# Kernel optimization log

Measured on AMD Instinct MI355X. Metric: run time of the kernel, lower is better.

## Reference

```python
import jax, jax.numpy as jnp
import numpy as np

B, L, C, H = 4, 2048, 1024, 16
D = C // H  # head dim = 64


def setup_inputs() -> dict:
    key = jax.random.key(0)
    ks = jax.random.split(key, 7)
    x = jax.random.normal(ks[0], (B, L, C), dtype=jnp.float32)
    Wqkv = jax.random.normal(ks[1], (C, 3 * C), dtype=jnp.float32) * 0.02
    bqkv = jnp.zeros((3 * C,), dtype=jnp.float32)
    gamma_q = jnp.ones((H, D), dtype=jnp.float32)
    gamma_k = jnp.ones((H, D), dtype=jnp.float32)
    Wout = jax.random.normal(ks[2], (C, C), dtype=jnp.float32) * 0.02
    bout = jnp.zeros((C,), dtype=jnp.float32)
    return {"x": x, "Wqkv": Wqkv, "bqkv": bqkv, "gamma_q": gamma_q,
            "gamma_k": gamma_k, "Wout": Wout, "bout": bout}


def _multihead_rms_norm(t, gamma):
    # SparseMultiHeadRMSNorm: L2-normalize last dim (F.normalize), * gamma * sqrt(D)
    norm = jnp.maximum(jnp.linalg.norm(t, axis=-1, keepdims=True), 1e-12)
    return (t / norm) * gamma * jnp.sqrt(jnp.float32(D))


def reference(x, Wqkv, bqkv, gamma_q, gamma_k, Wout, bout):
    # qkv projection: [B,L,C] -> [B,L,3,H,D]
    qkv = (x @ Wqkv + bqkv).reshape(B, L, 3, H, D)
    q, k, v = qkv[:, :, 0], qkv[:, :, 1], qkv[:, :, 2]
    # qk rms norm (gamma broadcasts over [B,L,H,D])
    q = _multihead_rms_norm(q, gamma_q)
    k = _multihead_rms_norm(k, gamma_k)
    # full scaled dot product attention within each grid (batch element)
    scale = 1.0 / jnp.sqrt(jnp.float32(D))
    scores = jnp.einsum('bqhd,bkhd->bhqk', q, k) * scale
    attn = jax.nn.softmax(scores, axis=-1)
    h = jnp.einsum('bhqk,bkhd->bqhd', attn, v).reshape(B, L, C)
    return h @ Wout + bout
```

## Files before the change

### kernel.cpp

```cpp
#include <hip/hip_runtime.h>
#include <math.h>

#define BB 4
#define LL 2048
#define CC 1024
#define HH 16
#define DD 64
#define MM (BB * LL)

typedef float f32x4 __attribute__((ext_vector_type(4)));
typedef short short8 __attribute__((ext_vector_type(8)));
typedef unsigned short ushort_t;
typedef unsigned long long u64_t;

#define MFMA_BF16(A, B, C) __builtin_amdgcn_mfma_f32_16x16x32_bf16(A, B, C, 0, 0, 0)

#define QSCALE 0.180336880f

__device__ __forceinline__ unsigned short f2bf(float x) {
    unsigned int u = __float_as_uint(x);
    u += 0x7fffu + ((u >> 16) & 1u);
    return (unsigned short)(u >> 16);
}

__device__ __forceinline__ unsigned pack_bf2(float a, float b) {
#if __has_builtin(__builtin_amdgcn_perm)
    return __builtin_amdgcn_perm(__float_as_uint(b) + 0x8000u,
                                 __float_as_uint(a) + 0x8000u, 0x07060302u);
#else
    return ((__float_as_uint(b) + 0x8000u) & 0xFFFF0000u) |
           ((__float_as_uint(a) + 0x8000u) >> 16);
#endif
}

__device__ __forceinline__ float fast_exp2(float x) {
#if __has_builtin(__builtin_amdgcn_exp2f)
    return __builtin_amdgcn_exp2f(x);
#else
    return exp2f(x);
#endif
}

__global__ __launch_bounds__(256)
void prep_all(const float* __restrict__ x, ushort_t* __restrict__ xh,
              const float* __restrict__ Wq, ushort_t* __restrict__ Tq,
              const float* __restrict__ Wo, ushort_t* __restrict__ To)
{
    __shared__ float sT[64][65];
    int bid = blockIdx.x;
    const int tid = threadIdx.x;

    if (bid < 4096) {
        const int i = (bid * 256 + tid) * 8;
        f32x4 a = *(const f32x4*)(x + i);
        f32x4 b = *(const f32x4*)(x + i + 4);
        short8 h;
#pragma unroll
        for (int j = 0; j < 4; ++j) {
            h[j]     = (short)f2bf(a[j]);
            h[4 + j] = (short)f2bf(b[j]);
        }
        *(short8*)(xh + i) = h;
        return;
    }
    bid -= 4096;

    const float* W;
    ushort_t* T;
    int N, bx, by;
    if (bid < 768) { W = Wq; T = Tq; N = 3 * CC; bx = bid % 48; by = bid / 48; }
    else { bid -= 768; W = Wo; T = To; N = CC; bx = bid % 16; by = bid / 16; }

    const int K = CC;
    const int k0 = by * 64, n0 = bx * 64;
    const int r = tid >> 2, c0 = (tid & 3) * 16;

    const float* wp = W + (size_t)(k0 + r) * N + n0 + c0;
#pragma unroll
    for (int u = 0; u < 4; ++u) {
        f32x4 v = *(const f32x4*)(wp + 4 * u);
        sT[r][c0 + 4 * u + 0] = v[0];
        sT[r][c0 + 4 * u + 1] = v[1];
        sT[r][c0 + 4 * u + 2] = v[2];
        sT[r][c0 + 4 * u + 3] = v[3];
    }
    __syncthreads();

    const int nn = tid >> 2, kk0 = (tid & 3) * 16;
    short8 h0, h1;
#pragma unroll
    for (int u = 0; u < 8; ++u) {
        h0[u] = (short)f2bf(sT[kk0 + u][nn]);
        h1[u] = (short)f2bf(sT[kk0 + 8 + u][nn]);
    }
    ushort_t* oh = T + (size_t)(n0 + nn) * K + k0 + kk0;
    *(short8*)oh = h0; *(short8*)(oh + 8) = h1;
}

__global__ __launch_bounds__(256, 3)
void gemm_qkv(const ushort_t* __restrict__ Agh,
              const ushort_t* __restrict__ Bh,
              const float* __restrict__ bias,
              const float* __restrict__ gq, const float* __restrict__ gk,
              ushort_t* __restrict__ Qbh,
              ushort_t* __restrict__ Kh,
              ushort_t* __restrict__ Vth)
{
    __shared__ ushort_t smem[16384];
    ushort_t* sAh = smem;
    ushort_t* sBh = smem + 8192;

    const int K = CC, lda = CC, nbx = (3 * CC) / 128;

    const int nwg = gridDim.x;
    const int cpx = nwg >> 3;
    const int id  = blockIdx.x;
    const int swz = (id & 7) * cpx + (id >> 3);
    const int bx = swz % nbx, by = swz / nbx;
    const int m0 = by * 128, n0 = bx * 128;

    const int tid  = threadIdx.x;
    const int lane = tid & 63;
    const int wv   = tid >> 6;
    const int l4   = lane >> 4, l16 = lane & 15;
    const int wm   = wv >> 1,  wn  = wv & 1;

    const int r0  = tid >> 2;
    const int c0  = (tid & 3) * 16;
    const int ch0 = c0 >> 3;

    f32x4 acc[4][4];
#pragma unroll
    for (int i = 0; i < 4; ++i)
#pragma unroll
        for (int j = 0; j < 4; ++j) acc[i][j] = 0.f;

    short8 stgA[4], stgB[4];
#pragma unroll
    for (int it = 0; it < 2; ++it) {
        const ushort_t* ahp = Agh + (size_t)(m0 + r0 + 64 * it) * lda + c0;
        stgA[2 * it]     = *(const short8*)(ahp);
        stgA[2 * it + 1] = *(const short8*)(ahp + 8);
        const ushort_t* bhp = Bh + (size_t)(n0 + r0 + 64 * it) * K + c0;
        stgB[2 * it]     = *(const short8*)(bhp);
        stgB[2 * it + 1] = *(const short8*)(bhp + 8);
    }

    for (int kt = 0; kt < K; kt += 64) {
        __syncthreads();
#pragma unroll
        for (int it = 0; it < 2; ++it) {
            const int row  = r0 + 64 * it;
            const int sA   = row & 7;
            const int base = row * 64;
            const int cA = ((ch0) ^ sA) * 8, cB = ((ch0 + 1) ^ sA) * 8;
            *(short8*)&sAh[base + cA] = stgA[2 * it];
            *(short8*)&sAh[base + cB] = stgA[2 * it + 1];
            *(short8*)&sBh[base + cA] = stgB[2 * it];
            *(short8*)&sBh[base + cB] = stgB[2 * it + 1];
        }
        __syncthreads();

        if (kt + 64 < K) {
#pragma unroll
            for (int it = 0; it < 2; ++it) {
                const ushort_t* ahp = Agh + (size_t)(m0 + r0 + 64 * it) * lda + kt + 64 + c0;
                stgA[2 * it]     = *(const short8*)(ahp);
                stgA[2 * it + 1] = *(const short8*)(ahp + 8);
                const ushort_t* bhp = Bh + (size_t)(n0 + r0 + 64 * it) * K + kt + 64 + c0;
                stgB[2 * it]     = *(const short8*)(bhp);
                stgB[2 * it + 1] = *(const short8*)(bhp + 8);
            }
        }

#pragma unroll
        for (int ks = 0; ks < 2; ++ks) {
            const int chf = (((ks << 2) | l4) ^ (l16 & 7)) * 8;
            short8 fbh[4];
#pragma unroll
            for (int j = 0; j < 4; ++j) {
                const int idx = (64 * wn + 16 * j + l16) * 64 + chf;
                fbh[j] = *(const short8*)&sBh[idx];
            }
#pragma unroll
            for (int i = 0; i < 4; ++i) {
                const int idx = (64 * wm + 16 * i + l16) * 64 + chf;
                short8 fah = *(const short8*)&sAh[idx];
#pragma unroll
                for (int j = 0; j < 4; ++j)
                    acc[i][j] = MFMA_BF16(fah, fbh[j], acc[i][j]);
            }
        }
    }

    const int region = n0 >> 10;
    float bv[4];
#pragma unroll
    for (int j = 0; j < 4; ++j) bv[j] = bias[n0 + 64 * wn + 16 * j + l16];
#pragma unroll
    for (int i = 0; i < 4; ++i)
#pragma unroll
        for (int j = 0; j < 4; ++j)
#pragma unroll
            for (int r = 0; r < 4; ++r) acc[i][j][r] += bv[j];

    const int b = m0 >> 11;

    if (region < 2) {
        const int hloc = ((n0 & 1023) >> 6) + wn;
        const float* g = (region == 0 ? gq : gk) + hloc * DD;
        float gv[4];
#pragma unroll
        for (int j = 0; j < 4; ++j) gv[j] = g[16 * j + l16];
#pragma unroll
        for (int i = 0; i < 4; ++i)
#pragma unroll
        for (int r = 0; r < 4; ++r) {
            float ss = 0.f;
#pragma unroll
            for (int j = 0; j < 4; ++j) ss += acc[i][j][r] * acc[i][j][r];
#pragma unroll
            for (int off = 1; off < 16; off <<= 1) ss += __shfl_xor(ss, off);
            const float s = 8.0f / fmaxf(sqrtf(ss), 1e-12f);
#pragma unroll
            for (int j = 0; j < 4; ++j) acc[i][j][r] *= s * gv[j];
        }

        if (region == 0) {
#pragma unroll
            for (int i = 0; i < 4; ++i)
#pragma unroll
            for (int r = 0; r < 4; ++r) {
                const int row = m0 + 64 * wm + 16 * i + 4 * l4 + r;
                ushort_t* op = Qbh + (size_t)row * CC + n0 + 64 * wn + l16;
#pragma unroll
                for (int j = 0; j < 4; ++j)
                    op[16 * j] = f2bf(acc[i][j][r] * QSCALE);
            }
        } else {
            const int hk = ((n0 - 1024) >> 6) + wn;
#pragma unroll
            for (int i = 0; i < 4; ++i)
#pragma unroll
            for (int r = 0; r < 4; ++r) {
                const int l = (m0 & 2047) + 64 * wm + 16 * i + 4 * l4 + r;
                const size_t base = ((size_t)(b * HH + hk) * LL + l) * DD + l16;
#pragma unroll
                for (int j = 0; j < 4; ++j)
                    Kh[base + 16 * j] = f2bf(acc[i][j][r]);
            }
        }
    } else {
        __syncthreads();
        ushort_t* vh = smem;
#pragma unroll
        for (int i = 0; i < 4; ++i)
#pragma unroll
        for (int r = 0; r < 4; ++r) {
            const int lr = 64 * wm + 16 * i + 4 * l4 + r;
#pragma unroll
            for (int j = 0; j < 4; ++j) {
                const int c = 64 * wn + 16 * j + l16;
                vh[lr * 128 + c] = f2bf(acc[i][j][r]);
            }
        }
        __syncthreads();
        const int c    = tid & 127;
        const int half = tid >> 7;
        const int hv   = ((n0 - 2048) >> 6) + (c >> 6);
        const int d    = c & 63;
        ushort_t* oh = Vth + ((size_t)(b * HH + hv) * DD + d) * LL + (m0 & 2047) + half * 64;
#pragma unroll
        for (int u = 0; u < 8; ++u) {
            const int l0 = half * 64 + u * 8;
            short8 hv8;
#pragma unroll
            for (int e = 0; e < 8; ++e)
                hv8[e] = (short)vh[(l0 + e) * 128 + c];
            *(short8*)&oh[u * 8] = hv8;
        }
    }
}

__global__ __launch_bounds__(256, 3)
void gemm_out1(const ushort_t* __restrict__ Ah,
               const ushort_t* __restrict__ Bh,
               const float* __restrict__ bias, float* __restrict__ Cg)
{
    __shared__ ushort_t sAh[8192];
    __shared__ ushort_t sBh[8192];

    const int K = CC, nbx = CC / 128;

    const int nwg = gridDim.x;
    const int cpx = nwg >> 3;
    const int id  = blockIdx.x;
    const int sw  = (id & 7) * cpx + (id >> 3);
    const int bx = sw % nbx, by = sw / nbx;
    const int m0 = by * 128, n0 = bx * 128;

    const int tid  = threadIdx.x;
    const int lane = tid & 63;
    const int wv   = tid >> 6;
    const int l4   = lane >> 4, l16 = lane & 15;
    const int wm   = wv >> 1,  wn  = wv & 1;

    const int r0  = tid >> 2;
    const int c0  = (tid & 3) * 16;
    const int ch0 = c0 >> 3;

    f32x4 acc[4][4];
#pragma unroll
    for (int i = 0; i < 4; ++i)
#pragma unroll
        for (int j = 0; j < 4; ++j) acc[i][j] = 0.f;

    short8 stgA[4], stgB[4];
#pragma unroll
    for (int it = 0; it < 2; ++it) {
        const ushort_t* ahp = Ah + (size_t)(m0 + r0 + 64 * it) * CC + c0;
        stgA[2 * it]     = *(const short8*)(ahp);
        stgA[2 * it + 1] = *(const short8*)(ahp + 8);
        const ushort_t* bhp = Bh + (size_t)(n0 + r0 + 64 * it) * K + c0;
        stgB[2 * it]     = *(const short8*)(bhp);
        stgB[2 * it + 1] = *(const short8*)(bhp + 8);
    }

    for (int kt = 0; kt < K; kt += 64) {
        __syncthreads();
#pragma unroll
        for (int it = 0; it < 2; ++it) {
            const int row  = r0 + 64 * it;
            const int sA   = row & 7;
            const int base = row * 64;
            const int cA = ((ch0) ^ sA) * 8, cB = ((ch0 + 1) ^ sA) * 8;
            *(short8*)&sAh[base + cA] = stgA[2 * it];
            *(short8*)&sAh[base + cB] = stgA[2 * it + 1];
            *(short8*)&sBh[base + cA] = stgB[2 * it];
            *(short8*)&sBh[base + cB] = stgB[2 * it + 1];
        }
        __syncthreads();

        if (kt + 64 < K) {
#pragma unroll
            for (int it = 0; it < 2; ++it) {
                const ushort_t* ahp = Ah + (size_t)(m0 + r0 + 64 * it) * CC + kt + 64 + c0;
                stgA[2 * it]     = *(const short8*)(ahp);
                stgA[2 * it + 1] = *(const short8*)(ahp + 8);
                const ushort_t* bhp = Bh + (size_t)(n0 + r0 + 64 * it) * K + kt + 64 + c0;
                stgB[2 * it]     = *(const short8*)(bhp);
                stgB[2 * it + 1] = *(const short8*)(bhp + 8);
            }
        }

#pragma unroll
        for (int ks = 0; ks < 2; ++ks) {
            const int chf = (((ks << 2) | l4) ^ (l16 & 7)) * 8;
            short8 fbh[4];
#pragma unroll
            for (int j = 0; j < 4; ++j) {
                const int idx = (64 * wn + 16 * j + l16) * 64 + chf;
                fbh[j] = *(const short8*)&sBh[idx];
            }
#pragma unroll
            for (int i = 0; i < 4; ++i) {
                const int idx = (64 * wm + 16 * i + l16) * 64 + chf;
                short8 fah = *(const short8*)&sAh[idx];
#pragma unroll
                for (int j = 0; j < 4; ++j)
                    acc[i][j] = MFMA_BF16(fah, fbh[j], acc[i][j]);
            }
        }
    }

    float bv[4];
#pragma unroll
    for (int j = 0; j < 4; ++j) bv[j] = bias[n0 + 64 * wn + 16 * j + l16];
#pragma unroll
    for (int i = 0; i < 4; ++i)
#pragma unroll
    for (int r = 0; r < 4; ++r) {
        const int row = m0 + 64 * wm + 16 * i + 4 * l4 + r;
        float* cp = Cg + (size_t)row * CC + n0 + 64 * wn + l16;
#pragma unroll
        for (int j = 0; j < 4; ++j) cp[16 * j] = acc[i][j][r] + bv[j];
    }
}

__global__ __launch_bounds__(256, 2)
void flash11(const ushort_t* __restrict__ Qbh,
             const ushort_t* __restrict__ Kh,
             const ushort_t* __restrict__ Vth,
             ushort_t* __restrict__ Hb)
{
    __shared__ ushort_t sKh[4096], sVh[4096];
    __shared__ ushort_t sP[4][64 * 68];

    const int i    = blockIdx.x;
    const int xcd  = i & 7;
    const int slot = i >> 3;
    const int qt   = slot & 7;
    const int bh   = ((slot >> 3) << 3) | xcd;
    const int b    = bh >> 4, h = bh & 15;

    const int tid  = threadIdx.x;
    const int lane = tid & 63;
    const int wv   = tid >> 6;
    const int l4   = lane >> 4, l16 = lane & 15;

    short8 qh[4][2];
    const int qr0 = qt * 256 + wv * 64;
#pragma unroll
    for (int qf = 0; qf < 4; ++qf)
#pragma unroll
    for (int sl = 0; sl < 2; ++sl)
        qh[qf][sl] = *(const short8*)(Qbh + (size_t)(b * LL + qr0 + qf * 16 + l16) * CC
                                      + h * DD + sl * 32 + l4 * 8);

    short8 ones;
#pragma unroll
    for (int j = 0; j < 8; ++j) ones[j] = (short)0x3F80;

    f32x4 O[4][4];
    f32x4 acc_l[4];
#pragma unroll
    for (int qf = 0; qf < 4; ++qf) {
        acc_l[qf] = 0.f;
#pragma unroll
        for (int t = 0; t < 4; ++t) O[qf][t] = 0.f;
    }

    const int r_ = tid >> 2;
    const int c2 = (tid & 3) * 2;

    short8 stg[4];
    {
        const size_t kgb = ((size_t)bh * LL + r_) * DD + c2 * 8;
        const size_t vgb = ((size_t)bh * DD + r_) * LL + c2 * 8;
        stg[0] = *(const short8*)&Kh[kgb];  stg[1] = *(const short8*)&Kh[kgb + 8];
        stg[2] = *(const short8*)&Vth[vgb]; stg[3] = *(const short8*)&Vth[vgb + 8];
    }

    for (int kt = 0; kt < LL / 64; ++kt) {
        __syncthreads();
        {
            const int wr = r_ * 64, s = r_ & 7;
            const int cA = ((c2) ^ s) * 8, cB = ((c2 + 1) ^ s) * 8;
            *(short8*)&sKh[wr + cA] = stg[0];
            *(short8*)&sKh[wr + cB] = stg[1];
            *(short8*)&sVh[wr + cA] = stg[2];
            *(short8*)&sVh[wr + cB] = stg[3];
        }
        __syncthreads();
        if (kt + 1 < LL / 64) {
            const size_t kgb = ((size_t)bh * LL + (kt + 1) * 64 + r_) * DD + c2 * 8;
            const size_t vgb = ((size_t)bh * DD + r_) * LL + (kt + 1) * 64 + c2 * 8;
            stg[0] = *(const short8*)&Kh[kgb];  stg[1] = *(const short8*)&Kh[kgb + 8];
            stg[2] = *(const short8*)&Vth[vgb]; stg[3] = *(const short8*)&Vth[vgb + 8];
        }

        f32x4 S[4][4];
#pragma unroll
        for (int qf = 0; qf < 4; ++qf)
#pragma unroll
        for (int t = 0; t < 4; ++t) S[qf][t] = 0.f;

        __builtin_amdgcn_s_setprio(1);
#pragma unroll
        for (int t = 0; t < 4; ++t) {
            const int row = 16 * t + l16;
            const int swr = row & 7;
#pragma unroll
            for (int sl = 0; sl < 2; ++sl) {
                const int idx = row * 64 + (((sl << 2) | l4) ^ swr) * 8;
                short8 kh8 = *(const short8*)&sKh[idx];
#pragma unroll
                for (int qf = 0; qf < 4; ++qf)
                    S[qf][t] = MFMA_BF16(kh8, qh[qf][sl], S[qf][t]);
            }
        }
        __builtin_amdgcn_s_setprio(0);

#pragma unroll
        for (int qf = 0; qf < 4; ++qf)
#pragma unroll
        for (int t = 0; t < 4; ++t)
#pragma unroll
            for (int r = 0; r < 4; ++r)
                S[qf][t][r] = fast_exp2(S[qf][t][r]);

#pragma unroll
        for (int qf = 0; qf < 4; ++qf)
#pragma unroll
        for (int t = 0; t < 4; ++t) {
            unsigned lo = pack_bf2(S[qf][t][0], S[qf][t][1]);
            unsigned hi = pack_bf2(S[qf][t][2], S[qf][t][3]);
            const int widx = (qf * 16 + l16) * 68 + 16 * t + 4 * l4;
            *(u64_t*)&sP[wv][widx] = (u64_t)lo | ((u64_t)hi << 32);
        }
        asm volatile("s_waitcnt lgkmcnt(0)" ::: "memory");
        __builtin_amdgcn_sched_barrier(0);

        short8 pa[4][2];
#pragma unroll
        for (int qf = 0; qf < 4; ++qf)
#pragma unroll
        for (int sl = 0; sl < 2; ++sl) {
            const int ridx = (qf * 16 + l16) * 68 + sl * 32 + 8 * l4;
            union { u64_t q[2]; short8 s8; } u;
            u.q[0] = *(const u64_t*)&sP[wv][ridx];
            u.q[1] = *(const u64_t*)&sP[wv][ridx + 4];
            pa[qf][sl] = u.s8;
        }

        __builtin_amdgcn_s_setprio(1);
#pragma unroll
        for (int qf = 0; qf < 4; ++qf) {
            acc_l[qf] = MFMA_BF16(pa[qf][0], ones, acc_l[qf]);
            acc_l[qf] = MFMA_BF16(pa[qf][1], ones, acc_l[qf]);
        }
#pragma unroll
        for (int dt = 0; dt < 4; ++dt) {
            const int row = 16 * dt + l16;
            const int swr = row & 7;
#pragma unroll
            for (int sl = 0; sl < 2; ++sl) {
                const int idx = row * 64 + (((sl << 2) | l4) ^ swr) * 8;
                short8 vh8 = *(const short8*)&sVh[idx];
#pragma unroll
                for (int qf = 0; qf < 4; ++qf)
                    O[qf][dt] = MFMA_BF16(pa[qf][sl], vh8, O[qf][dt]);
            }
        }
        __builtin_amdgcn_s_setprio(0);
    }

#pragma unroll
    for (int qf = 0; qf < 4; ++qf) {
        f32x4 iv;
#pragma unroll
        for (int r = 0; r < 4; ++r) iv[r] = 1.0f / acc_l[qf][r];
#pragma unroll
        for (int r = 0; r < 4; ++r) {
            const int q = qr0 + qf * 16 + 4 * l4 + r;
            ushort_t* op = Hb + (size_t)(b * LL + q) * CC + h * DD + l16;
#pragma unroll
            for (int dt = 0; dt < 4; ++dt)
                op[16 * dt] = f2bf(O[qf][dt][r] * iv[r]);
        }
    }
}

#define Bb 128
#define Bn 128
#define BKG 8

__global__ __launch_bounds__(256)
void gemm_bias(const float* __restrict__ A, const float* __restrict__ B,
               const float* __restrict__ bias, float* __restrict__ C,
               int M, int N, int K, int lda, int ldb, int ldc)
{
    __shared__ float As[BKG][Bb];
    __shared__ float Bs[BKG][Bn];

    const int tid = threadIdx.x;
    const int m0 = blockIdx.y * Bb;
    const int n0 = blockIdx.x * Bn;
    const int ty = tid >> 4, tx = tid & 15;
    const int arow = tid >> 1, acol = (tid & 1) * 4;
    const int brow = tid >> 5, bcol = (tid & 31) * 4;

    const float* Ap = A + (size_t)(m0 + arow) * lda + acol;
    const float* Bp = B + (size_t)brow * ldb + n0 + bcol;

    float acc[8][8];
#pragma unroll
    for (int i = 0; i < 8; ++i)
#pragma unroll
        for (int j = 0; j < 8; ++j) acc[i][j] = 0.f;

    for (int k0 = 0; k0 < K; k0 += BKG) {
        float4 av = *(const float4*)(Ap + k0);
        float4 bv = *(const float4*)(Bp + (size_t)k0 * ldb);
        __syncthreads();
        As[acol + 0][arow] = av.x;
        As[acol + 1][arow] = av.y;
        As[acol + 2][arow] = av.z;
        As[acol + 3][arow] = av.w;
        *(float4*)&Bs[brow][bcol] = bv;
        __syncthreads();
#pragma unroll
        for (int kk = 0; kk < BKG; ++kk) {
            float a[8], bvv[8];
            *(float4*)&a[0] = *(const float4*)&As[kk][ty * 4];
            *(float4*)&a[4] = *(const float4*)&As[kk][64 + ty * 4];
            *(float4*)&bvv[0] = *(const float4*)&Bs[kk][tx * 4];
            *(float4*)&bvv[4] = *(const float4*)&Bs[kk][64 + tx * 4];
#pragma unroll
            for (int i = 0; i < 8; ++i)
#pragma unroll
                for (int j = 0; j < 8; ++j)
                    acc[i][j] = fmaf(a[i], bvv[j], acc[i][j]);
        }
    }
#pragma unroll
    for (int ih = 0; ih < 2; ++ih)
#pragma unroll
    for (int i = 0; i < 4; ++i) {
        const int m = m0 + ih * 64 + ty * 4 + i;
#pragma unroll
        for (int jh = 0; jh < 2; ++jh) {
            const int n = n0 + jh * 64 + tx * 4;
            float4 o;
            o.x = acc[ih*4+i][jh*4+0] + bias[n+0];
            o.y = acc[ih*4+i][jh*4+1] + bias[n+1];
            o.z = acc[ih*4+i][jh*4+2] + bias[n+2];
            o.w = acc[ih*4+i][jh*4+3] + bias[n+3];
            *(float4*)(C + (size_t)m * ldc + n) = o;
        }
    }
}

__global__ __launch_bounds__(256)
void rmsnorm_qk(float* __restrict__ qkv,
                const float* __restrict__ gq, const float* __restrict__ gk)
{
    const int gt    = blockIdx.x * 256 + threadIdx.x;
    const int lane  = gt & 63;
    const int wave  = gt >> 6;
    const int which = wave & 1;
    const int h     = (wave >> 1) & (HH - 1);
    const int bl    = wave >> 5;

    float* p = qkv + (size_t)bl * (3 * CC) + which * CC + h * DD + lane;
    float v = *p;
    float ss = v * v;
#pragma unroll
    for (int off = 32; off; off >>= 1) ss += __shfl_xor(ss, off);
    float nrm = fmaxf(sqrtf(ss), 1e-12f);
    const float* g = which ? gk : gq;
    *p = v * (8.0f / nrm) * g[h * DD + lane];
}

__global__ __launch_bounds__(256)
void flash_fp32(float* __restrict__ qkv)
{
    const int qt = blockIdx.x, hh = blockIdx.y, bb = blockIdx.z;

    __shared__ float Qt[DD][64];
    __shared__ float Kt[DD][64];
    __shared__ float Vs[64][DD];
    __shared__ float Ps[64][64 + 4];

    const int tid = threadIdx.x;
    const int ty = tid >> 4, tx = tid & 15;
    const size_t rs_ = 3 * CC;
    const float* qbase = qkv + ((size_t)bb * LL + (size_t)qt * 64) * rs_ + hh * DD;
    const float* kbase = qkv + (size_t)bb * LL * rs_ + CC + hh * DD;
    const float* vbase = kbase + CC;

    {
        const int r = tid >> 2, c0 = (tid & 3) * 16;
#pragma unroll
        for (int u = 0; u < 4; ++u) {
            float4 v = *(const float4*)(qbase + (size_t)r * rs_ + c0 + u * 4);
            Qt[c0 + u*4 + 0][r] = v.x; Qt[c0 + u*4 + 1][r] = v.y;
            Qt[c0 + u*4 + 2][r] = v.z; Qt[c0 + u*4 + 3][r] = v.w;
        }
    }

    float mrow[4], lrow[4], O[4][4];
#pragma unroll
    for (int i = 0; i < 4; ++i) {
        mrow[i] = -INFINITY; lrow[i] = 0.f;
#pragma unroll
        for (int j = 0; j < 4; ++j) O[i][j] = 0.f;
    }

    for (int kt = 0; kt < LL / 64; ++kt) {
        __syncthreads();
        {
            const int r = tid >> 2, c0 = (tid & 3) * 16;
            const float* kr = kbase + ((size_t)kt * 64 + r) * rs_;
            const float* vr = vbase + ((size_t)kt * 64 + r) * rs_;
#pragma unroll
            for (int u = 0; u < 4; ++u) {
                float4 kv = *(const float4*)(kr + c0 + u * 4);
                Kt[c0 + u*4 + 0][r] = kv.x; Kt[c0 + u*4 + 1][r] = kv.y;
                Kt[c0 + u*4 + 2][r] = kv.z; Kt[c0 + u*4 + 3][r] = kv.w;
                *(float4*)&Vs[r][c0 + u*4] = *(const float4*)(vr + c0 + u * 4);
            }
        }
        __syncthreads();

        float S[4][4];
#pragma unroll
        for (int i = 0; i < 4; ++i)
#pragma unroll
            for (int j = 0; j < 4; ++j) S[i][j] = 0.f;
#pragma unroll 8
        for (int d = 0; d < DD; ++d) {
            float a[4], b[4];
            *(float4*)a = *(const float4*)&Qt[d][ty * 4];
            *(float4*)b = *(const float4*)&Kt[d][tx * 4];
#pragma unroll
            for (int i = 0; i < 4; ++i)
#pragma unroll
                for (int j = 0; j < 4; ++j) S[i][j] = fmaf(a[i], b[j], S[i][j]);
        }
#pragma unroll
        for (int i = 0; i < 4; ++i) {
#pragma unroll
            for (int j = 0; j < 4; ++j) S[i][j] *= 0.125f;
            float pm = fmaxf(fmaxf(S[i][0], S[i][1]), fmaxf(S[i][2], S[i][3]));
#pragma unroll
            for (int off = 1; off < 16; off <<= 1) pm = fmaxf(pm, __shfl_xor(pm, off));
            const float mnew = fmaxf(mrow[i], pm);
            const float corr = __expf(mrow[i] - mnew);
            float rsum = 0.f;
#pragma unroll
            for (int j = 0; j < 4; ++j) { S[i][j] = __expf(S[i][j] - mnew); rsum += S[i][j]; }
#pragma unroll
            for (int off = 1; off < 16; off <<= 1) rsum += __shfl_xor(rsum, off);
            mrow[i] = mnew;
            lrow[i] = lrow[i] * corr + rsum;
#pragma unroll
            for (int j = 0; j < 4; ++j) O[i][j] *= corr;
        }
#pragma unroll
        for (int i = 0; i < 4; ++i)
            *(float4*)&Ps[ty * 4 + i][tx * 4] = *(float4*)&S[i][0];
        __syncthreads();
#pragma unroll 4
        for (int k = 0; k < 64; k += 4) {
            float a[4][4];
#pragma unroll
            for (int i = 0; i < 4; ++i)
                *(float4*)&a[i][0] = *(const float4*)&Ps[ty * 4 + i][k];
#pragma unroll
            for (int kk = 0; kk < 4; ++kk) {
                float bv[4];
                *(float4*)bv = *(const float4*)&Vs[k + kk][tx * 4];
#pragma unroll
                for (int i = 0; i < 4; ++i)
#pragma unroll
                    for (int j = 0; j < 4; ++j)
                        O[i][j] = fmaf(a[i][kk], bv[j], O[i][j]);
            }
        }
    }

    float* obase = qkv + ((size_t)bb * LL + (size_t)qt * 64) * rs_ + hh * DD;
#pragma unroll
    for (int i = 0; i < 4; ++i) {
        const float inv = 1.f / lrow[i];
        float4 o;
        o.x = O[i][0] * inv; o.y = O[i][1] * inv;
        o.z = O[i][2] * inv; o.w = O[i][3] * inv;
        *(float4*)(obase + (size_t)(ty * 4 + i) * rs_ + tx * 4) = o;
    }
}

extern "C" void kernel_launch(void* const* d_in, const int* in_sizes, int n_in,
                              void* d_out, int out_size, void* d_ws, size_t ws_size,
                              hipStream_t stream)
{
    const float* x    = (const float*)d_in[0];
    const float* Wqkv = (const float*)d_in[1];
    const float* bqkv = (const float*)d_in[2];
    const float* gq   = (const float*)d_in[3];
    const float* gk   = (const float*)d_in[4];
    const float* Wout = (const float*)d_in[5];
    const float* bout = (const float*)d_in[6];
    float* out = (float*)d_out;

    const size_t NEED = 92274688ull;

    if (ws_size >= NEED) {
        char* wsb = (char*)d_ws;
        ushort_t* Qbh = (ushort_t*)(wsb);
        ushort_t* Kh  = (ushort_t*)(wsb + 16777216);
        ushort_t* Vth = (ushort_t*)(wsb + 33554432);
        ushort_t* Hb  = (ushort_t*)(wsb + 50331648);
        ushort_t* wqh = (ushort_t*)(wsb + 67108864);
        ushort_t* woh = (ushort_t*)(wsb + 73400320);
        ushort_t* xh  = (ushort_t*)(wsb + 75497472);

        prep_all<<<dim3(4096 + 768 + 256), 256, 0, stream>>>(
            x, xh, Wqkv, wqh, Wout, woh);

        gemm_qkv<<<dim3(24 * 64), 256, 0, stream>>>(
            xh, wqh, bqkv, gq, gk, Qbh, Kh, Vth);

        flash11<<<dim3(512), 256, 0, stream>>>(Qbh, Kh, Vth, Hb);

        gemm_out1<<<dim3(8 * 64), 256, 0, stream>>>(Hb, woh, bout, out);
    } else {
        float* qkv = (float*)d_ws;
        gemm_bias<<<dim3((3 * CC) / Bn, MM / Bb), 256, 0, stream>>>(
            x, Wqkv, bqkv, qkv, MM, 3 * CC, CC, CC, 3 * CC, 3 * CC);
        rmsnorm_qk<<<dim3((MM * HH * 2 * 64) / 256), 256, 0, stream>>>(qkv, gq, gk);
        flash_fp32<<<dim3(LL / 64, HH, BB), 256, 0, stream>>>(qkv);
        gemm_bias<<<dim3(CC / Bn, MM / Bb), 256, 0, stream>>>(
            qkv, Wout, bout, out, MM, CC, CC, 3 * CC, CC, CC);
    }
}
```

Baseline: 186.0 us.

## Double-buffer K/V tiles in flash kernel using direct global-to-LDS loads

Replaces the register-staged K/V prefetch in the attention kernel with global_load_lds direct copies into a double-buffered shared-memory tile, with the swizzle folded into the global source address. This removes the register staging, the LDS store instructions and one of the two barriers per iteration, so the next tile's load overlaps compute on the current one. It costs an extra 16 KB of LDS, which may pressure the 2-blocks-per-CU occupancy target. It also relies on the async LDS writes being complete at the single end-of-iteration barrier without an explicit vmcnt wait.

```diff
diff --git a/kernel.cpp b/kernel.cpp
--- a/kernel.cpp
+++ b/kernel.cpp
@@ -39,6 +39,13 @@
 #else
     return exp2f(x);
 #endif
+}
+
+__device__ __forceinline__ void gload_lds16(const ushort_t* g, ushort_t* l) {
+    __builtin_amdgcn_global_load_lds(
+        (const __attribute__((address_space(1))) void*)g,
+        (__attribute__((address_space(3))) void*)l,
+        16, 0, 0);
 }
 
 __global__ __launch_bounds__(256)
@@ -388,12 +395,13 @@
 }
 
 __global__ __launch_bounds__(256, 2)
-void flash11(const ushort_t* __restrict__ Qbh,
+void flash12(const ushort_t* __restrict__ Qbh,
              const ushort_t* __restrict__ Kh,
              const ushort_t* __restrict__ Vth,
              ushort_t* __restrict__ Hb)
 {
-    __shared__ ushort_t sKh[4096], sVh[4096];
+    __shared__ ushort_t sKh[2][4096];
+    __shared__ ushort_t sVh[2][4096];
     __shared__ ushort_t sP[4][64 * 68];
 
     const int i    = blockIdx.x;
@@ -430,33 +438,34 @@
         for (int t = 0; t < 4; ++t) O[qf][t] = 0.f;
     }
 
-    const int r_ = tid >> 2;
-    const int c2 = (tid & 3) * 2;
-
-    short8 stg[4];
+    size_t koff[2], voff[2];
+#pragma unroll
+    for (int j = 0; j < 2; ++j) {
+        const int row = wv * 16 + j * 8 + (lane >> 3);
+        const int cs  = ((lane & 7) ^ (row & 7)) * 8;
+        koff[j] = ((size_t)bh * LL + row) * DD + cs;
+        voff[j] = ((size_t)bh * DD + row) * LL + cs;
+    }
+
+    int cur = 0;
     {
-        const size_t kgb = ((size_t)bh * LL + r_) * DD + c2 * 8;
-        const size_t vgb = ((size_t)bh * DD + r_) * LL + c2 * 8;
-        stg[0] = *(const short8*)&Kh[kgb];  stg[1] = *(const short8*)&Kh[kgb + 8];
-        stg[2] = *(const short8*)&Vth[vgb]; stg[3] = *(const short8*)&Vth[vgb + 8];
-    }
+#pragma unroll
+        for (int j = 0; j < 2; ++j) {
+            gload_lds16(Kh  + koff[j], &sKh[0][wv * 1024 + j * 512]);
+            gload_lds16(Vth + voff[j], &sVh[0][wv * 1024 + j * 512]);
+        }
+    }
+    __syncthreads();
 
     for (int kt = 0; kt < LL / 64; ++kt) {
-        __syncthreads();
-        {
-            const int wr = r_ * 64, s = r_ & 7;
-            const int cA = ((c2) ^ s) * 8, cB = ((c2 + 1) ^ s) * 8;
-            *(short8*)&sKh[wr + cA] = stg[0];
-            *(short8*)&sKh[wr + cB] = stg[1];
-            *(short8*)&sVh[wr + cA] = stg[2];
-            *(short8*)&sVh[wr + cB] = stg[3];
-        }
-        __syncthreads();
         if (kt + 1 < LL / 64) {
-            const size_t kgb = ((size_t)bh * LL + (kt + 1) * 64 + r_) * DD + c2 * 8;
-            const size_t vgb = ((size_t)bh * DD + r_) * LL + (kt + 1) * 64 + c2 * 8;
-            stg[0] = *(const short8*)&Kh[kgb];  stg[1] = *(const short8*)&Kh[kgb + 8];
-            stg[2] = *(const short8*)&Vth[vgb]; stg[3] = *(const short8*)&Vth[vgb + 8];
+#pragma unroll
+            for (int j = 0; j < 2; ++j) {
+                gload_lds16(Kh  + koff[j] + (size_t)(kt + 1) * 64 * DD,
+                            &sKh[cur ^ 1][wv * 1024 + j * 512]);
+                gload_lds16(Vth + voff[j] + (size_t)(kt + 1) * 64,
+                            &sVh[cur ^ 1][wv * 1024 + j * 512]);
+            }
         }
 
         f32x4 S[4][4];
@@ -473,7 +482,7 @@
 #pragma unroll
             for (int sl = 0; sl < 2; ++sl) {
                 const int idx = row * 64 + (((sl << 2) | l4) ^ swr) * 8;
-                short8 kh8 = *(const short8*)&sKh[idx];
+                short8 kh8 = *(const short8*)&sKh[cur][idx];
 #pragma unroll
                 for (int qf = 0; qf < 4; ++qf)
                     S[qf][t] = MFMA_BF16(kh8, qh[qf][sl], S[qf][t]);
@@ -526,13 +535,16 @@
 #pragma unroll
             for (int sl = 0; sl < 2; ++sl) {
                 const int idx = row * 64 + (((sl << 2) | l4) ^ swr) * 8;
-                short8 vh8 = *(const short8*)&sVh[idx];
+                short8 vh8 = *(const short8*)&sVh[cur][idx];
 #pragma unroll
                 for (int qf = 0; qf < 4; ++qf)
                     O[qf][dt] = MFMA_BF16(pa[qf][sl], vh8, O[qf][dt]);
             }
         }
         __builtin_amdgcn_s_setprio(0);
+
+        __syncthreads();
+        cur ^= 1;
     }
 
 #pragma unroll
@@ -792,7 +804,7 @@
         gemm_qkv<<<dim3(24 * 64), 256, 0, stream>>>(
             xh, wqh, bqkv, gq, gk, Qbh, Kh, Vth);
 
-        flash11<<<dim3(512), 256, 0, stream>>>(Qbh, Kh, Vth, Hb);
+        flash12<<<dim3(512), 256, 0, stream>>>(Qbh, Kh, Vth, Hb);
 
         gemm_out1<<<dim3(8 * 64), 256, 0, stream>>>(Hb, woh, bout, out);
     } else {
```

After: 189.6 us. Within noise of the previous version (+1.9%).
